# Optimization experiments

Hardware: AMD Instinct MI355X
Metric: run time of the kernel (lower is better)

Reference implementation:

```python
import jax, jax.numpy as jnp
import numpy as np

B, N, C, H = 8, 1024, 1024, 16
DH = C // H
SCALE = DH ** -0.5
EPS = 1e-6


def layernorm(x, g, b):
    m = jnp.mean(x, axis=-1, keepdims=True)
    v = jnp.mean(jnp.square(x - m), axis=-1, keepdims=True)
    return (x - m) * jax.lax.rsqrt(v + EPS) * g + b


def setup_inputs() -> dict:
    key = jax.random.key(0)
    ks = jax.random.split(key, 5)
    w = 0.02  # init std for weights, keeps activations sane
    return {
        "x": jax.random.normal(ks[0], (B, N, C), jnp.float32),
        "qkv_w": jax.random.normal(ks[1], (C, 3 * C), jnp.float32) * w,
        "qkv_b": jnp.zeros((3 * C,), jnp.float32),
        "proj_w": jax.random.normal(ks[2], (C, C), jnp.float32) * w,
        "proj_b": jnp.zeros((C,), jnp.float32),
        "n1_g": jnp.ones((C,), jnp.float32),
        "n1_b": jnp.zeros((C,), jnp.float32),
        "fc1_w": jax.random.normal(ks[3], (C, 4 * C), jnp.float32) * w,
        "fc1_b": jnp.zeros((4 * C,), jnp.float32),
        "fc2_w": jax.random.normal(ks[4], (4 * C, C), jnp.float32) * w,
        "fc2_b": jnp.zeros((C,), jnp.float32),
        "n2_g": jnp.ones((C,), jnp.float32),
        "n2_b": jnp.zeros((C,), jnp.float32),
    }


def reference(x, qkv_w, qkv_b, proj_w, proj_b, n1_g, n1_b,
              fc1_w, fc1_b, fc2_w, fc2_b, n2_g, n2_b):
    # --- manual multi-head attention (timm-style, materializes BxHxNxN) ---
    qkv = x @ qkv_w + qkv_b                                  # [B,N,3C]
    qkv = qkv.reshape(B, N, 3, H, DH).transpose(2, 0, 3, 1, 4)  # [3,B,H,N,DH]
    q, k, v = qkv[0], qkv[1], qkv[2]
    attn = jax.nn.softmax(jnp.einsum('bhnd,bhmd->bhnm', q, k) * SCALE, axis=-1)
    y = jnp.einsum('bhnm,bhmd->bhnd', attn, v)               # [B,H,N,DH]
    y = y.transpose(0, 2, 1, 3).reshape(B, N, C)
    y = y @ proj_w + proj_b                                  # attention output replaces x
    # --- NOTE: unusual block wiring, faithful to source ---
    # x = attn_out; x = x + norm1(x); x = x + norm2(mlp(x))
    y = y + layernorm(y, n1_g, n1_b)
    h = jax.nn.gelu(y @ fc1_w + fc1_b, approximate=False)    # timm Mlp: fc1 -> GELU -> fc2
    h = h @ fc2_w + fc2_b
    y = y + layernorm(h, n2_g, n2_b)
    return y
```

## Files before the change

### kernel.cpp

```cpp
#include <hip/hip_runtime.h>
#include <hip/hip_bf16.h>
#include <math.h>

typedef __bf16 bf16;
typedef __bf16 bf16x8 __attribute__((ext_vector_type(8)));
typedef float f32x4 __attribute__((ext_vector_type(4)));

__device__ __forceinline__ int swz_idx(int row, int col) {
    return ((row) << 6) + (((((col) >> 3) ^ ((row) & 7)) << 3) | ((col) & 7));
}
#define LDS_SWZ8(row, c8) ((((row)) << 6) + ((((c8) ^ ((row) & 7))) << 3))

__device__ __forceinline__ void gload_lds16(const bf16* g, bf16* l) {
    __builtin_amdgcn_global_load_lds(
        (const __attribute__((address_space(1))) void*)g,
        (__attribute__((address_space(3))) void*)l,
        16, 0, 0);
}

template <int ROWS>
__device__ __forceinline__ void stage_swz(const bf16* __restrict__ src, long rstride,
                                          bf16* lds, int tid) {
#pragma unroll
    for (int pass = 0; pass < ROWS / 32; ++pass) {
        int e = pass * 2048 + tid * 8;
        int r = e >> 6;
        int c8 = (e >> 3) & 7;
        int sc8 = c8 ^ (r & 7);
        gload_lds16(src + (long)r * rstride + sc8 * 8, lds + e);
    }
}

__device__ __forceinline__ float bf2f(unsigned short u) {
    unsigned int v = (unsigned int)u << 16;
    return __builtin_bit_cast(float, v);
}
__device__ __forceinline__ short f2bf_s(float f) {
    return (short)__builtin_bit_cast(unsigned short, (bf16)f);
}

__global__ void transpose_cvt(const float* __restrict__ src, bf16* __restrict__ dst,
                              int R, int C) {
    __shared__ float tile[32][33];
    int bx = blockIdx.x * 32;
    int by = blockIdx.y * 32;
    int tx = threadIdx.x, ty = threadIdx.y;
#pragma unroll
    for (int j = 0; j < 32; j += 8)
        tile[ty + j][tx] = src[(long)(by + ty + j) * C + bx + tx];
    __syncthreads();
#pragma unroll
    for (int j = 0; j < 32; j += 8)
        dst[(long)(bx + ty + j) * R + by + tx] = (bf16)tile[tx][ty + j];
}

__global__ void cvt_bf16_kernel(const float* __restrict__ src, bf16* __restrict__ dst,
                                long n) {
    long i = ((long)blockIdx.x * blockDim.x + threadIdx.x) * 4;
    if (i < n) {
        float4 v = *(const float4*)(src + i);
        short4 pk;
        pk.x = f2bf_s(v.x); pk.y = f2bf_s(v.y); pk.z = f2bf_s(v.z); pk.w = f2bf_s(v.w);
        *(short4*)(dst + i) = pk;
    }
}

template <int MODE>
__global__ __launch_bounds__(256, 2)
void gemm_bt(const bf16* __restrict__ A, const bf16* __restrict__ Bt,
             const float* __restrict__ bias,
             float* __restrict__ Cf, bf16* __restrict__ Cb0,
             bf16* __restrict__ Cb1, bf16* __restrict__ Cb2,
             int M, int N, int K) {
    __shared__ __align__(16) bf16 lsA[256 * 64];
    __shared__ __align__(16) bf16 lsB[128 * 64];

    const int nwg = gridDim.x * gridDim.y;
    const int lin = blockIdx.y * gridDim.x + blockIdx.x;
    const int swz = (lin & 7) * (nwg >> 3) + (lin >> 3);
    const int bx = swz % gridDim.x, by = swz / gridDim.x;

    const int tid = threadIdx.x;
    const int lane = tid & 63;
    const int w = tid >> 6;
    const int wm = w >> 1, wn = w & 1;
    const int l15 = lane & 15, l4 = lane >> 4;
    const int row0 = by * 256;
    const int col0 = bx * 128;

    f32x4 acc[8][4] = {};

    for (int k0 = 0; k0 < K; k0 += 64) {
        stage_swz<256>(A + (long)row0 * K + k0, K, lsA, tid);
        stage_swz<128>(Bt + (long)col0 * K + k0, K, lsB, tid);
        __syncthreads();
#pragma unroll
        for (int kk = 0; kk < 2; ++kk) {
            int c8 = kk * 4 + l4;
            bf16x8 aF[8], bF[4];
#pragma unroll
            for (int mt = 0; mt < 8; ++mt)
                aF[mt] = *(const bf16x8*)(&lsA[LDS_SWZ8(wm * 128 + mt * 16 + l15, c8)]);
#pragma unroll
            for (int nt = 0; nt < 4; ++nt)
                bF[nt] = *(const bf16x8*)(&lsB[LDS_SWZ8(wn * 64 + nt * 16 + l15, c8)]);
#pragma unroll
            for (int mt = 0; mt < 8; ++mt)
#pragma unroll
                for (int nt = 0; nt < 4; ++nt)
                    acc[mt][nt] = __builtin_amdgcn_mfma_f32_16x16x32_bf16(
                        aF[mt], bF[nt], acc[mt][nt], 0, 0, 0);
        }
        __syncthreads();
    }

#pragma unroll
    for (int mt = 0; mt < 8; ++mt) {
#pragma unroll
        for (int nt = 0; nt < 4; ++nt) {
            int colb = col0 + wn * 64 + nt * 16 + l15;
            float bv = bias[colb];
#pragma unroll
            for (int i = 0; i < 4; ++i) {
                int row = row0 + wm * 128 + mt * 16 + l4 * 4 + i;
                int col = colb;
                float v = acc[mt][nt][i] + bv;
                if (MODE == 0) {
                    int b = row >> 10, nn = row & 1023;
                    int s = col >> 10, rem = col & 1023;
                    int h = rem >> 6, d = rem & 63;
                    long bh = (long)b * 16 + h;
                    if (s == 0)      Cb0[(bh * 1024 + nn) * 64 + d] = (bf16)(v * 0.1803368881f);
                    else if (s == 1) Cb1[(bh * 1024 + nn) * 64 + d] = (bf16)v;
                    else             Cb2[(bh * 64 + d) * 1024 + nn] = (bf16)v;
                } else if (MODE == 1) {
                    Cb0[(long)row * N + col] = (bf16)v;
                } else if (MODE == 2) {
                    float g = 0.5f * v * (1.0f + erff(v * 0.70710678118f));
                    Cb0[(long)row * N + col] = (bf16)g;
                } else {
                    Cf[(long)row * N + col] = v;
                }
            }
        }
    }
}

__global__ __launch_bounds__(256, 2)
void attn_flash(const bf16* __restrict__ Q, const bf16* __restrict__ Kv,
                const bf16* __restrict__ Vt, bf16* __restrict__ Y) {
    __shared__ __align__(16) bf16 lsK[2][64 * 64];
    __shared__ __align__(16) bf16 lsV[2][64 * 64];
    __shared__ __align__(16) bf16 lsP[4][16 * 64];

    const int tid = threadIdx.x;
    const int lane = tid & 63;
    const int w = tid >> 6;
    const int l15 = lane & 15, l4 = lane >> 4;
    const int bh = blockIdx.y;
    const int b = bh >> 4, h = bh & 15;
    const int q0 = blockIdx.x * 64;

    const bf16* qp = Q + ((long)bh * 1024 + q0 + w * 16 + l15) * 64;
    bf16x8 qa[2];
    qa[0] = *(const bf16x8*)(qp + 8 * l4);
    qa[1] = *(const bf16x8*)(qp + 32 + 8 * l4);

    const bf16* kbase = Kv + (long)bh * 1024 * 64;
    const bf16* vbase = Vt + (long)bh * 64 * 1024;

    float lsum[4] = {0.f, 0.f, 0.f, 0.f};
    f32x4 oacc[4] = {};

    stage_swz<64>(kbase, 64, lsK[0], tid);
    stage_swz<64>(vbase, 1024, lsV[0], tid);
    __syncthreads();

    for (int t = 0; t < 16; ++t) {
        const int cur = t & 1;
        if (t < 15) {
            int kv0 = (t + 1) * 64;
            stage_swz<64>(kbase + (long)kv0 * 64, 64, lsK[cur ^ 1], tid);
            stage_swz<64>(vbase + kv0, 1024, lsV[cur ^ 1], tid);
        }

        f32x4 s[4] = {};
        __builtin_amdgcn_s_setprio(1);
#pragma unroll
        for (int kk = 0; kk < 2; ++kk) {
            int c8 = kk * 4 + l4;
#pragma unroll
            for (int nt = 0; nt < 4; ++nt) {
                bf16x8 kb = *(const bf16x8*)(&lsK[cur][LDS_SWZ8(nt * 16 + l15, c8)]);
                s[nt] = __builtin_amdgcn_mfma_f32_16x16x32_bf16(qa[kk], kb, s[nt], 0, 0, 0);
            }
        }
        __builtin_amdgcn_s_setprio(0);

#pragma unroll
        for (int i = 0; i < 4; ++i) {
            int prow = l4 * 4 + i;
#pragma unroll
            for (int nt = 0; nt < 4; ++nt) {
                float p = exp2f(s[nt][i]);
                lsum[i] += p;
                lsP[w][swz_idx(prow, nt * 16 + l15)] = (bf16)p;
            }
        }
        __builtin_amdgcn_sched_barrier(0);
        asm volatile("s_waitcnt lgkmcnt(0)" ::: "memory");
        __builtin_amdgcn_sched_barrier(0);

        __builtin_amdgcn_s_setprio(1);
#pragma unroll
        for (int kk = 0; kk < 2; ++kk) {
            int c8 = kk * 4 + l4;
            bf16x8 pa = *(const bf16x8*)(&lsP[w][LDS_SWZ8(l15, c8)]);
#pragma unroll
            for (int nt = 0; nt < 4; ++nt) {
                bf16x8 vb = *(const bf16x8*)(&lsV[cur][LDS_SWZ8(nt * 16 + l15, c8)]);
                oacc[nt] = __builtin_amdgcn_mfma_f32_16x16x32_bf16(pa, vb, oacc[nt], 0, 0, 0);
            }
        }
        __builtin_amdgcn_s_setprio(0);
        __syncthreads();
    }

#pragma unroll
    for (int i = 0; i < 4; ++i) {
#pragma unroll
        for (int off = 1; off < 16; off <<= 1)
            lsum[i] += __shfl_xor(lsum[i], off);
    }

#pragma unroll
    for (int i = 0; i < 4; ++i) {
        float rinv = 1.0f / lsum[i];
        int row = q0 + w * 16 + l4 * 4 + i;
#pragma unroll
        for (int nt = 0; nt < 4; ++nt) {
            int d = nt * 16 + l15;
            Y[((long)b * 1024 + row) * 1024 + h * 64 + d] = (bf16)(oacc[nt][i] * rinv);
        }
    }
}

__device__ __forceinline__ float block_reduce_sum(float v, float* sm) {
#pragma unroll
    for (int off = 1; off < 64; off <<= 1) v += __shfl_xor(v, off);
    int w = threadIdx.x >> 6;
    if ((threadIdx.x & 63) == 0) sm[w] = v;
    __syncthreads();
    v = sm[0] + sm[1] + sm[2] + sm[3];
    __syncthreads();
    return v;
}

__global__ __launch_bounds__(256)
void res_ln(const bf16* __restrict__ Yin, bf16* __restrict__ Yout,
            const float* __restrict__ g, const float* __restrict__ beta) {
    __shared__ float sm[4];
    const long row = blockIdx.x;
    const int t = threadIdx.x;
    short4 raw = *(const short4*)(Yin + row * 1024 + t * 4);
    float x0 = bf2f((unsigned short)raw.x), x1 = bf2f((unsigned short)raw.y);
    float x2 = bf2f((unsigned short)raw.z), x3 = bf2f((unsigned short)raw.w);
    float s = x0 + x1 + x2 + x3;
    s = block_reduce_sum(s, sm);
    float mean = s * (1.0f / 1024.0f);
    float d0 = x0 - mean, d1 = x1 - mean, d2 = x2 - mean, d3 = x3 - mean;
    float sq = d0 * d0 + d1 * d1 + d2 * d2 + d3 * d3;
    sq = block_reduce_sum(sq, sm);
    float rs = rsqrtf(sq * (1.0f / 1024.0f) + 1e-6f);
    float4 gg = *(const float4*)(g + t * 4);
    float4 bb = *(const float4*)(beta + t * 4);
    short4 pk;
    pk.x = f2bf_s(x0 + d0 * rs * gg.x + bb.x);
    pk.y = f2bf_s(x1 + d1 * rs * gg.y + bb.y);
    pk.z = f2bf_s(x2 + d2 * rs * gg.z + bb.z);
    pk.w = f2bf_s(x3 + d3 * rs * gg.w + bb.w);
    *(short4*)(Yout + row * 1024 + t * 4) = pk;
}

__global__ __launch_bounds__(256)
void final_ln(float* __restrict__ Hf, const bf16* __restrict__ Yres,
              const float* __restrict__ g, const float* __restrict__ beta) {
    __shared__ float sm[4];
    const long row = blockIdx.x;
    float* p = Hf + row * 1024;
    const int t = threadIdx.x;
    float4 x = *(const float4*)(p + t * 4);
    float s = x.x + x.y + x.z + x.w;
    s = block_reduce_sum(s, sm);
    float mean = s * (1.0f / 1024.0f);
    float d0 = x.x - mean, d1 = x.y - mean, d2 = x.z - mean, d3 = x.w - mean;
    float sq = d0 * d0 + d1 * d1 + d2 * d2 + d3 * d3;
    sq = block_reduce_sum(sq, sm);
    float rs = rsqrtf(sq * (1.0f / 1024.0f) + 1e-6f);
    float4 gg = *(const float4*)(g + t * 4);
    float4 bb = *(const float4*)(beta + t * 4);
    short4 yr = *(const short4*)(Yres + row * 1024 + t * 4);
    float4 o;
    o.x = bf2f((unsigned short)yr.x) + d0 * rs * gg.x + bb.x;
    o.y = bf2f((unsigned short)yr.y) + d1 * rs * gg.y + bb.y;
    o.z = bf2f((unsigned short)yr.z) + d2 * rs * gg.z + bb.z;
    o.w = bf2f((unsigned short)yr.w) + d3 * rs * gg.w + bb.w;
    *(float4*)(p + t * 4) = o;
}

extern "C" void kernel_launch(void* const* d_in, const int* in_sizes, int n_in,
                              void* d_out, int out_size, void* d_ws, size_t ws_size,
                              hipStream_t stream) {
    const float* x      = (const float*)d_in[0];
    const float* qkv_w  = (const float*)d_in[1];
    const float* qkv_b  = (const float*)d_in[2];
    const float* proj_w = (const float*)d_in[3];
    const float* proj_b = (const float*)d_in[4];
    const float* n1_g   = (const float*)d_in[5];
    const float* n1_b   = (const float*)d_in[6];
    const float* fc1_w  = (const float*)d_in[7];
    const float* fc1_b  = (const float*)d_in[8];
    const float* fc2_w  = (const float*)d_in[9];
    const float* fc2_b  = (const float*)d_in[10];
    const float* n2_g   = (const float*)d_in[11];
    const float* n2_b   = (const float*)d_in[12];

    char* ws = (char*)d_ws;
    const long MB = 1l << 20;
    bf16*  qkvT   = (bf16*)(ws + 0 * MB);
    bf16*  projT  = (bf16*)(ws + 6 * MB);
    bf16*  fc1T   = (bf16*)(ws + 8 * MB);
    bf16*  fc2T   = (bf16*)(ws + 16 * MB);
    bf16*  xbf    = (bf16*)(ws + 24 * MB);
    bf16*  yattn  = (bf16*)(ws + 24 * MB);
    bf16*  qb     = (bf16*)(ws + 40 * MB);
    bf16*  kb     = (bf16*)(ws + 56 * MB);
    bf16*  vtb    = (bf16*)(ws + 72 * MB);
    bf16*  yprojb = (bf16*)(ws + 40 * MB);
    bf16*  yresb  = (bf16*)(ws + 72 * MB);
    bf16*  h1     = (bf16*)(ws + 88 * MB);
    float* outf   = (float*)d_out;

    dim3 tb(32, 8);
    transpose_cvt<<<dim3(3072 / 32, 1024 / 32), tb, 0, stream>>>(qkv_w, qkvT, 1024, 3072);
    transpose_cvt<<<dim3(1024 / 32, 1024 / 32), tb, 0, stream>>>(proj_w, projT, 1024, 1024);
    transpose_cvt<<<dim3(4096 / 32, 1024 / 32), tb, 0, stream>>>(fc1_w, fc1T, 1024, 4096);
    transpose_cvt<<<dim3(1024 / 32, 4096 / 32), tb, 0, stream>>>(fc2_w, fc2T, 4096, 1024);
    cvt_bf16_kernel<<<8192, 256, 0, stream>>>(x, xbf, 8388608);

    gemm_bt<0><<<dim3(3072 / 128, 8192 / 256), 256, 0, stream>>>(
        xbf, qkvT, qkv_b, nullptr, qb, kb, vtb, 8192, 3072, 1024);
    attn_flash<<<dim3(1024 / 64, 128), 256, 0, stream>>>(qb, kb, vtb, yattn);
    gemm_bt<1><<<dim3(1024 / 128, 8192 / 256), 256, 0, stream>>>(
        yattn, projT, proj_b, nullptr, yprojb, nullptr, nullptr, 8192, 1024, 1024);
    res_ln<<<8192, 256, 0, stream>>>(yprojb, yresb, n1_g, n1_b);
    gemm_bt<2><<<dim3(4096 / 128, 8192 / 256), 256, 0, stream>>>(
        yresb, fc1T, fc1_b, nullptr, h1, nullptr, nullptr, 8192, 4096, 1024);
    gemm_bt<3><<<dim3(1024 / 128, 8192 / 256), 256, 0, stream>>>(
        h1, fc2T, fc2_b, outf, nullptr, nullptr, nullptr, 8192, 1024, 4096);
    final_ln<<<8192, 256, 0, stream>>>(outf, yresb, n2_g, n2_b);
}
```

Baseline: 431.3 us.

## Shrink GEMM tiles, fuse preprocessing kernels, remap attention grid for locality

Cuts the GEMM block tile from 256x128 to 128x128 and raises the launch-bounds occupancy target to 4 blocks per CU, doubling the grid. It also merges the four weight transposes and the x conversion into one launch, and flattens the attention grid so that consecutive blocks are spread across (batch, head) groups in an XCD-aware order. Smaller tiles give more waves and better load balance but lower the arithmetic intensity per tile and add global traffic. The occupancy hint may also force register limits.

```diff
diff --git a/kernel.cpp b/kernel.cpp
--- a/kernel.cpp
+++ b/kernel.cpp
@@ -39,40 +39,50 @@
     return (short)__builtin_bit_cast(unsigned short, (bf16)f);
 }
 
-__global__ void transpose_cvt(const float* __restrict__ src, bf16* __restrict__ dst,
-                              int R, int C) {
-    __shared__ float tile[32][33];
-    int bx = blockIdx.x * 32;
-    int by = blockIdx.y * 32;
-    int tx = threadIdx.x, ty = threadIdx.y;
-#pragma unroll
-    for (int j = 0; j < 32; j += 8)
-        tile[ty + j][tx] = src[(long)(by + ty + j) * C + bx + tx];
-    __syncthreads();
-#pragma unroll
-    for (int j = 0; j < 32; j += 8)
-        dst[(long)(bx + ty + j) * R + by + tx] = (bf16)tile[tx][ty + j];
-}
-
-__global__ void cvt_bf16_kernel(const float* __restrict__ src, bf16* __restrict__ dst,
-                                long n) {
-    long i = ((long)blockIdx.x * blockDim.x + threadIdx.x) * 4;
-    if (i < n) {
-        float4 v = *(const float4*)(src + i);
+__global__ __launch_bounds__(256)
+void preprocess_all(const float* __restrict__ qkv_w, const float* __restrict__ proj_w,
+                    const float* __restrict__ fc1_w, const float* __restrict__ fc2_w,
+                    const float* __restrict__ x,
+                    bf16* __restrict__ qkvT, bf16* __restrict__ projT,
+                    bf16* __restrict__ fc1T, bf16* __restrict__ fc2T,
+                    bf16* __restrict__ xbf) {
+    const int id = blockIdx.x;
+    const int tid = threadIdx.x;
+
+    if (id >= 12288) {
+        long i = ((long)(id - 12288) * 256 + tid) * 4;
+        float4 v = *(const float4*)(x + i);
         short4 pk;
         pk.x = f2bf_s(v.x); pk.y = f2bf_s(v.y); pk.z = f2bf_s(v.z); pk.w = f2bf_s(v.w);
-        *(short4*)(dst + i) = pk;
-    }
+        *(short4*)(xbf + i) = pk;
+        return;
+    }
+
+    const float* src; bf16* dst; int R, C, bx, by;
+    if (id < 3072)      { src = qkv_w; dst = qkvT; R = 1024; C = 3072; bx = id % 96;  by = id / 96; }
+    else if (id < 4096) { int t = id - 3072; src = proj_w; dst = projT; R = 1024; C = 1024; bx = t % 32;  by = t / 32; }
+    else if (id < 8192) { int t = id - 4096; src = fc1_w;  dst = fc1T;  R = 1024; C = 4096; bx = t % 128; by = t / 128; }
+    else                { int t = id - 8192; src = fc2_w;  dst = fc2T;  R = 4096; C = 1024; bx = t % 32;  by = t / 32; }
+
+    __shared__ float tile[32][33];
+    const int tx = tid & 31, ty = tid >> 5;
+#pragma unroll
+    for (int j = 0; j < 32; j += 8)
+        tile[ty + j][tx] = src[(long)(by * 32 + ty + j) * C + bx * 32 + tx];
+    __syncthreads();
+#pragma unroll
+    for (int j = 0; j < 32; j += 8)
+        dst[(long)(bx * 32 + ty + j) * R + by * 32 + tx] = (bf16)tile[tx][ty + j];
 }
 
 template <int MODE>
-__global__ __launch_bounds__(256, 2)
+__global__ __launch_bounds__(256, 4)
 void gemm_bt(const bf16* __restrict__ A, const bf16* __restrict__ Bt,
              const float* __restrict__ bias,
              float* __restrict__ Cf, bf16* __restrict__ Cb0,
              bf16* __restrict__ Cb1, bf16* __restrict__ Cb2,
              int M, int N, int K) {
-    __shared__ __align__(16) bf16 lsA[256 * 64];
+    __shared__ __align__(16) bf16 lsA[128 * 64];
     __shared__ __align__(16) bf16 lsB[128 * 64];
 
     const int nwg = gridDim.x * gridDim.y;
@@ -85,44 +95,44 @@
     const int w = tid >> 6;
     const int wm = w >> 1, wn = w & 1;
     const int l15 = lane & 15, l4 = lane >> 4;
-    const int row0 = by * 256;
+    const int row0 = by * 128;
     const int col0 = bx * 128;
 
-    f32x4 acc[8][4] = {};
+    f32x4 acc[4][4] = {};
 
     for (int k0 = 0; k0 < K; k0 += 64) {
-        stage_swz<256>(A + (long)row0 * K + k0, K, lsA, tid);
+        stage_swz<128>(A + (long)row0 * K + k0, K, lsA, tid);
         stage_swz<128>(Bt + (long)col0 * K + k0, K, lsB, tid);
         __syncthreads();
 #pragma unroll
         for (int kk = 0; kk < 2; ++kk) {
             int c8 = kk * 4 + l4;
-            bf16x8 aF[8], bF[4];
-#pragma unroll
-            for (int mt = 0; mt < 8; ++mt)
-                aF[mt] = *(const bf16x8*)(&lsA[LDS_SWZ8(wm * 128 + mt * 16 + l15, c8)]);
+            bf16x8 af[4], bfr[4];
+#pragma unroll
+            for (int mt = 0; mt < 4; ++mt)
+                af[mt] = *(const bf16x8*)(&lsA[LDS_SWZ8(wm * 64 + mt * 16 + l15, c8)]);
 #pragma unroll
             for (int nt = 0; nt < 4; ++nt)
-                bF[nt] = *(const bf16x8*)(&lsB[LDS_SWZ8(wn * 64 + nt * 16 + l15, c8)]);
-#pragma unroll
-            for (int mt = 0; mt < 8; ++mt)
+                bfr[nt] = *(const bf16x8*)(&lsB[LDS_SWZ8(wn * 64 + nt * 16 + l15, c8)]);
+#pragma unroll
+            for (int mt = 0; mt < 4; ++mt)
 #pragma unroll
                 for (int nt = 0; nt < 4; ++nt)
                     acc[mt][nt] = __builtin_amdgcn_mfma_f32_16x16x32_bf16(
-                        aF[mt], bF[nt], acc[mt][nt], 0, 0, 0);
+                        af[mt], bfr[nt], acc[mt][nt], 0, 0, 0);
         }
         __syncthreads();
     }
 
 #pragma unroll
-    for (int mt = 0; mt < 8; ++mt) {
+    for (int mt = 0; mt < 4; ++mt) {
 #pragma unroll
         for (int nt = 0; nt < 4; ++nt) {
             int colb = col0 + wn * 64 + nt * 16 + l15;
             float bv = bias[colb];
 #pragma unroll
             for (int i = 0; i < 4; ++i) {
-                int row = row0 + wm * 128 + mt * 16 + l4 * 4 + i;
+                int row = row0 + wm * 64 + mt * 16 + l4 * 4 + i;
                 int col = colb;
                 float v = acc[mt][nt][i] + bv;
                 if (MODE == 0) {
@@ -146,20 +156,24 @@
     }
 }
 
-__global__ __launch_bounds__(256, 2)
+__global__ __launch_bounds__(256, 4)
 void attn_flash(const bf16* __restrict__ Q, const bf16* __restrict__ Kv,
                 const bf16* __restrict__ Vt, bf16* __restrict__ Y) {
     __shared__ __align__(16) bf16 lsK[2][64 * 64];
     __shared__ __align__(16) bf16 lsV[2][64 * 64];
     __shared__ __align__(16) bf16 lsP[4][16 * 64];
 
+    const int raw = blockIdx.x;
+    const int c   = raw & 7;
+    const int g   = raw >> 3;
+    const int bh  = c * 16 + (g >> 4);
+    const int q0  = (g & 15) * 64;
+
     const int tid = threadIdx.x;
     const int lane = tid & 63;
     const int w = tid >> 6;
     const int l15 = lane & 15, l4 = lane >> 4;
-    const int bh = blockIdx.y;
     const int b = bh >> 4, h = bh & 15;
-    const int q0 = blockIdx.x * 64;
 
     const bf16* qp = Q + ((long)bh * 1024 + q0 + w * 16 + l15) * 64;
     bf16x8 qa[2];
@@ -341,22 +355,18 @@
     bf16*  h1     = (bf16*)(ws + 88 * MB);
     float* outf   = (float*)d_out;
 
-    dim3 tb(32, 8);
-    transpose_cvt<<<dim3(3072 / 32, 1024 / 32), tb, 0, stream>>>(qkv_w, qkvT, 1024, 3072);
-    transpose_cvt<<<dim3(1024 / 32, 1024 / 32), tb, 0, stream>>>(proj_w, projT, 1024, 1024);
-    transpose_cvt<<<dim3(4096 / 32, 1024 / 32), tb, 0, stream>>>(fc1_w, fc1T, 1024, 4096);
-    transpose_cvt<<<dim3(1024 / 32, 4096 / 32), tb, 0, stream>>>(fc2_w, fc2T, 4096, 1024);
-    cvt_bf16_kernel<<<8192, 256, 0, stream>>>(x, xbf, 8388608);
-
-    gemm_bt<0><<<dim3(3072 / 128, 8192 / 256), 256, 0, stream>>>(
+    preprocess_all<<<20480, 256, 0, stream>>>(qkv_w, proj_w, fc1_w, fc2_w, x,
+                                              qkvT, projT, fc1T, fc2T, xbf);
+
+    gemm_bt<0><<<dim3(3072 / 128, 8192 / 128), 256, 0, stream>>>(
         xbf, qkvT, qkv_b, nullptr, qb, kb, vtb, 8192, 3072, 1024);
-    attn_flash<<<dim3(1024 / 64, 128), 256, 0, stream>>>(qb, kb, vtb, yattn);
-    gemm_bt<1><<<dim3(1024 / 128, 8192 / 256), 256, 0, stream>>>(
+    attn_flash<<<2048, 256, 0, stream>>>(qb, kb, vtb, yattn);
+    gemm_bt<1><<<dim3(1024 / 128, 8192 / 128), 256, 0, stream>>>(
         yattn, projT, proj_b, nullptr, yprojb, nullptr, nullptr, 8192, 1024, 1024);
     res_ln<<<8192, 256, 0, stream>>>(yprojb, yresb, n1_g, n1_b);
-    gemm_bt<2><<<dim3(4096 / 128, 8192 / 256), 256, 0, stream>>>(
+    gemm_bt<2><<<dim3(4096 / 128, 8192 / 128), 256, 0, stream>>>(
         yresb, fc1T, fc1_b, nullptr, h1, nullptr, nullptr, 8192, 4096, 1024);
-    gemm_bt<3><<<dim3(1024 / 128, 8192 / 256), 256, 0, stream>>>(
+    gemm_bt<3><<<dim3(1024 / 128, 8192 / 128), 256, 0, stream>>>(
         h1, fc2T, fc2_b, outf, nullptr, nullptr, nullptr, 8192, 1024, 4096);
     final_ln<<<8192, 256, 0, stream>>>(outf, yresb, n2_g, n2_b);
 }
```

Result: faster. 358.5 us (-16.9%).
